# Kernel tuning notes

Hardware: AMD Instinct MI355X
Metric: run time of the kernel (lower is better)

## Reference

```python
import jax, jax.numpy as jnp
import numpy as np

B, L, DIM, K, V = 512, 200, 256, 2048, 100000


def setup_inputs() -> dict:
    key = jax.random.key(0)
    k1, k2, k3, k4, k5 = jax.random.split(key, 5)
    return {
        "history_item_ids": jax.random.randint(k1, (B, L), 0, V, dtype=jnp.int32),
        "history_item_masks": jax.random.randint(k2, (B, L), 0, 3, dtype=jnp.int32),
        "embedding_table": jax.random.normal(k3, (V, DIM), dtype=jnp.float32) * 0.1,
        "code_book": jax.random.normal(k4, (K, DIM), dtype=jnp.float32) * 0.1,
        "W_enc": jax.random.normal(k5, (2 * DIM, DIM), dtype=jnp.float32) * 0.05,
        "b_enc": jnp.zeros((DIM,), dtype=jnp.float32),
    }


def reference(history_item_ids, history_item_masks, embedding_table, code_book, W_enc, b_enc):
    # mask: valid history positions (>= 1)
    mask = (history_item_masks >= 1).astype(jnp.float32)            # [B, L]
    emb = embedding_table[history_item_ids] * mask[:, :, None]      # [B, L, D]
    # masked mean over history (eps matches the tf 1e-9)
    hist_mean = emb.sum(axis=1) / (mask.sum(axis=1, keepdims=True) + 1e-9)  # [B, D]
    # VQ quantization: pairwise squared distances, argmin, codebook gather
    flat = emb.reshape(-1, emb.shape[-1])                           # [B*L, D]
    distances = (
        jnp.sum(flat * flat, axis=1, keepdims=True)
        + jnp.sum(code_book * code_book, axis=1)
        - 2.0 * flat @ code_book.T
    )                                                               # [B*L, K]
    idx = jnp.argmin(distances, axis=1)                             # [B*L]
    vq = code_book[idx].reshape(emb.shape)                          # [B, L, D] (== one_hot @ code_book)
    vq_mean = vq.sum(axis=1) / mask.sum(axis=-1)[:, None]           # [B, D] (no eps in tf vqvae)
    x = jnp.concatenate([vq_mean, hist_mean], axis=-1)              # [B, 2D]
    return x @ W_enc + b_enc                                        # encoder dense -> [B, D]
```

## Files before the change

### kernel.cpp

```cpp
#include <hip/hip_runtime.h>
#include <hip/hip_bf16.h>
#include <cstddef>
#include <cstdint>

#define B_  512
#define L_  200
#define D_  256
#define K_  2048
#define BL_ (B_ * L_)

typedef __bf16 bf16x8 __attribute__((ext_vector_type(8)));
typedef float  f32x16 __attribute__((ext_vector_type(16)));

#define GL_LDS(g, l) __builtin_amdgcn_global_load_lds(                          \
    (const __attribute__((address_space(1))) void*)(g),                         \
    (__attribute__((address_space(3))) void*)(l), 16, 0, 0)

__device__ inline ushort f2bf(float f) {
    union { float f; uint u; } a; a.f = f;
    uint r = a.u + 0x7FFFu + ((a.u >> 16) & 1u);
    return (ushort)(r >> 16);
}

__global__ __launch_bounds__(256) void prep_kernel(const float* __restrict__ cb,
                                                   float* __restrict__ cnorm,
                                                   float* __restrict__ cnormR,
                                                   ushort* __restrict__ cbbf) {
    int code = (blockIdx.x * 256 + threadIdx.x) >> 6;
    int lane = threadIdx.x & 63;
    float4 v = ((const float4*)(cb + (size_t)code * D_))[lane];
    float s = v.x * v.x + v.y * v.y + v.z * v.z + v.w * v.w;
    #pragma unroll
    for (int off = 32; off; off >>= 1) s += __shfl_down(s, off);
    union { ushort us[4]; uint2 u2; } pk;
    pk.us[0] = f2bf(v.x); pk.us[1] = f2bf(v.y); pk.us[2] = f2bf(v.z); pk.us[3] = f2bf(v.w);
    ((uint2*)(cbbf + (size_t)code * D_))[lane] = pk.u2;
    if (lane == 0) {
        cnorm[code] = s;
        int r = code & 31;
        int h = (r >> 2) & 1;
        int j = (r & 3) | ((r >> 3) << 2);
        cnormR[(code & ~31) | (h << 4) | j] = s + 16.0f;
    }
}

struct CN4 { float4 a, b, c, d; };

__device__ inline CN4 ldcn(const float* p) {
    CN4 r;
    r.a = ((const float4*)p)[0];
    r.b = ((const float4*)p)[1];
    r.c = ((const float4*)p)[2];
    r.d = ((const float4*)p)[3];
    return r;
}

#define STAGE(CIDX, BUF) {                                                      \
    int wub = __builtin_amdgcn_readfirstlane((t >> 6) * 512);                   \
    _Pragma("unroll")                                                           \
    for (int i_ = 0; i_ < 8; ++i_) {                                            \
      int slot = wub + i_ * 64 + (t & 63);                                      \
      int n_ = slot >> 5, up_ = slot & 31;                                      \
      int u_ = up_ ^ (n_ & 7);                                                  \
      GL_LDS(cbbf + (((size_t)((cu << 10) + ((CIDX) << 5) + n_)) << 8) + (u_ << 3), \
             (char*)(BUF) + (size_t)(wub + i_ * 64) * 16);                      \
    } }

#define PROCSEL(BUF, NC, CN) {                                                  \
    f32x16 A0, A1;                                                              \
    A0[0]=(CN).a.x; A0[1]=(CN).a.y; A0[2]=(CN).a.z; A0[3]=(CN).a.w;             \
    A0[4]=(CN).b.x; A0[5]=(CN).b.y; A0[6]=(CN).b.z; A0[7]=(CN).b.w;             \
    A0[8]=(CN).c.x; A0[9]=(CN).c.y; A0[10]=(CN).c.z; A0[11]=(CN).c.w;           \
    A0[12]=(CN).d.x; A0[13]=(CN).d.y; A0[14]=(CN).d.z; A0[15]=(CN).d.w;         \
    A1 = A0;                                                                    \
    _Pragma("unroll")                                                           \
    for (int s_ = 0; s_ < 16; ++s_) {                                           \
      bf16x8 aF = *(const bf16x8*)((const char*)(BUF) +                         \
                    (((l31 << 5) + ((2 * s_ + h) ^ swz)) << 4));                \
      A0 = __builtin_amdgcn_mfma_f32_32x32x16_bf16(aF, bfrag[0][s_], A0, 0,0,0);\
      A1 = __builtin_amdgcn_mfma_f32_32x32x16_bf16(aF, bfrag[1][s_], A1, 0,0,0);\
    }                                                                           \
    uint sb_ = (uint)((cu << 10) + ((NC) << 5));                                \
    _Pragma("unroll")                                                           \
    for (int jp_ = 0; jp_ < 8; ++jp_) {                                         \
      int j0_ = 2 * jp_, j1_ = 2 * jp_ + 1;                                     \
      uint c0_ = sb_ + (uint)((j0_ & 3) + 8 * (j0_ >> 2));                      \
      uint c1_ = sb_ + (uint)((j1_ & 3) + 8 * (j1_ >> 2));                      \
      {                                                                         \
        uint ka = (__float_as_uint(A0[j0_]) & 0xFFFFF800u) | (c0_ + h4);        \
        uint kb = (__float_as_uint(A0[j1_]) & 0xFFFFF800u) | (c1_ + h4);        \
        uint lo = min(ka, kb), hi = max(ka, kb);                                \
        uint tt = max(b1a, lo);                                                 \
        b1a = min(b1a, lo);                                                     \
        b2a = min(min(b2a, tt), hi);                                            \
      }                                                                         \
      {                                                                         \
        uint ka = (__float_as_uint(A1[j0_]) & 0xFFFFF800u) | (c0_ + h4);        \
        uint kb = (__float_as_uint(A1[j1_]) & 0xFFFFF800u) | (c1_ + h4);        \
        uint lo = min(ka, kb), hi = max(ka, kb);                                \
        uint tt = max(b1b, lo);                                                 \
        b1b = min(b1b, lo);                                                     \
        b2b = min(min(b2b, tt), hi);                                            \
      }                                                                         \
    } }

__global__ __launch_bounds__(128, 2) void gemm_top2_kernel(
    const int* __restrict__ ids, const int* __restrict__ masks,
    const float* __restrict__ table, const ushort* __restrict__ cbbf,
    const float* __restrict__ cnormR, uint2* __restrict__ cand) {

  __shared__ ushort cbuf0[32 * 256];
  __shared__ ushort cbuf1[32 * 256];

  const int t    = threadIdx.x;
  const int lane = t & 63;
  const int l31  = lane & 31;
  const int h    = lane >> 5;
  const int w    = t >> 6;
  const int ptile = blockIdx.x >> 1;
  const int cu    = blockIdx.x & 1;
  const int swz  = l31 & 7;
  const uint h4  = (uint)(h << 2);

  bf16x8 bfrag[2][16];
  #pragma unroll
  for (int pt = 0; pt < 2; ++pt) {
    int pos = ptile * 128 + w * 64 + pt * 32 + l31;
    int id  = ids[pos];
    float m = (masks[pos] >= 1) ? -2.0f : 0.0f;
    const float* er = table + (size_t)id * D_ + 8 * h;
    #pragma unroll
    for (int s = 0; s < 16; ++s) {
      float4 x = *(const float4*)(er + 16 * s);
      float4 y = *(const float4*)(er + 16 * s + 4);
      bf16x8 b;
      b[0] = (__bf16)(x.x * m); b[1] = (__bf16)(x.y * m);
      b[2] = (__bf16)(x.z * m); b[3] = (__bf16)(x.w * m);
      b[4] = (__bf16)(y.x * m); b[5] = (__bf16)(y.y * m);
      b[6] = (__bf16)(y.z * m); b[7] = (__bf16)(y.w * m);
      bfrag[pt][s] = b;
    }
  }

  uint b1a = 0xFFFFFFFFu, b2a = 0xFFFFFFFFu;
  uint b1b = 0xFFFFFFFFu, b2b = 0xFFFFFFFFu;

  const float* cnh = cnormR + (cu << 10);
  CN4 cnA = ldcn(cnh + 0 * 32 + h * 16);
  STAGE(0, cbuf0);
  __syncthreads();

  #pragma unroll 1
  for (int nc = 0; nc < 32; nc += 2) {
    CN4 cnB = ldcn(cnh + (nc + 1) * 32 + h * 16);
    STAGE(nc + 1, cbuf1);
    PROCSEL(cbuf0, nc, cnA);
    __syncthreads();
    if (nc + 2 < 32) {
      cnA = ldcn(cnh + (nc + 2) * 32 + h * 16);
      STAGE(nc + 2, cbuf0);
    }
    PROCSEL(cbuf1, nc + 1, cnB);
    __syncthreads();
  }

  {
    uint ob1 = __shfl_xor(b1a, 32), ob2 = __shfl_xor(b2a, 32);
    uint m1 = min(b1a, ob1);
    uint m2 = min(min(max(b1a, ob1), b2a), ob2);
    if (h == 0) cand[(size_t)(ptile * 128 + w * 64 + 0 * 32 + l31) * 2 + cu] = make_uint2(m1, m2);
  }
  {
    uint ob1 = __shfl_xor(b1b, 32), ob2 = __shfl_xor(b2b, 32);
    uint m1 = min(b1b, ob1);
    uint m2 = min(min(max(b1b, ob1), b2b), ob2);
    if (h == 0) cand[(size_t)(ptile * 128 + w * 64 + 1 * 32 + l31) * 2 + cu] = make_uint2(m1, m2);
  }
}

#define SEG 5
#define PPB (L_ / SEG)
#define PPW (PPB / 4)

__global__ __launch_bounds__(256) void rescore_accum_kernel(
    const int* __restrict__ ids, const int* __restrict__ masks,
    const float* __restrict__ table, const float* __restrict__ cb,
    const float* __restrict__ cnorm, const uint4* __restrict__ cand,
    float* __restrict__ gacc, int* __restrict__ gcnt) {

    __shared__ float red_vq[4][D_];
    __shared__ float red_e[4][D_];
    __shared__ int   red_c[4];

    const int b   = blockIdx.x / SEG;
    const int seg = blockIdx.x % SEG;
    const int t = threadIdx.x;
    const int wv = t >> 6, lane = t & 63;

    float4 vqa = make_float4(0.f, 0.f, 0.f, 0.f);
    float4 ea  = make_float4(0.f, 0.f, 0.f, 0.f);
    int cnta = 0;

    #pragma unroll 2
    for (int i = 0; i < PPW; ++i) {
        int l = seg * PPB + wv * PPW + i;
        int u = b * L_ + l;
        uint4 k4 = cand[u];
        uint g1 = min(k4.x, k4.z);
        uint g2 = min(min(max(k4.x, k4.z), k4.y), k4.w);
        int ia = (int)(g1 & 0x7FFu), ib2 = (int)(g2 & 0x7FFu);
        int lo = min(ia, ib2), hi = max(ia, ib2);
        int id = ids[u];
        bool mv = (masks[u] >= 1);
        float m = mv ? 1.0f : 0.0f;
        float4 e = ((const float4*)(table + (size_t)id * D_))[lane];
        e.x *= m; e.y *= m; e.z *= m; e.w *= m;
        float4 a  = ((const float4*)(cb + (size_t)lo * D_))[lane];
        float4 bb = ((const float4*)(cb + (size_t)hi * D_))[lane];
        float s1 = fmaf(e.x, a.x,  fmaf(e.y, a.y,  fmaf(e.z, a.z,  e.w * a.w)));
        float s2 = fmaf(e.x, bb.x, fmaf(e.y, bb.y, fmaf(e.z, bb.z, e.w * bb.w)));
        #pragma unroll
        for (int off = 32; off; off >>= 1) {
            s1 += __shfl_xor(s1, off);
            s2 += __shfl_xor(s2, off);
        }
        float d1 = cnorm[lo] - 2.0f * s1;
        float d2 = cnorm[hi] - 2.0f * s2;
        bool sel = (d2 < d1);
        float4 ch = sel ? bb : a;
        vqa.x += ch.x; vqa.y += ch.y; vqa.z += ch.z; vqa.w += ch.w;
        ea.x += e.x; ea.y += e.y; ea.z += e.z; ea.w += e.w;
        cnta += mv ? 1 : 0;
    }

    *(float4*)&red_vq[wv][lane * 4] = vqa;
    *(float4*)&red_e[wv][lane * 4]  = ea;
    if (lane == 0) red_c[wv] = cnta;
    __syncthreads();

    float vs = red_vq[0][t] + red_vq[1][t] + red_vq[2][t] + red_vq[3][t];
    float es = red_e[0][t] + red_e[1][t] + red_e[2][t] + red_e[3][t];
    atomicAdd(&gacc[(size_t)b * (2 * D_) + t], vs);
    atomicAdd(&gacc[(size_t)b * (2 * D_) + D_ + t], es);
    if (t == 0) atomicAdd(&gcnt[b], red_c[0] + red_c[1] + red_c[2] + red_c[3]);
}

__global__ __launch_bounds__(256) void dense_kernel(
    const float* __restrict__ gacc, const int* __restrict__ gcnt,
    const float* __restrict__ W, const float* __restrict__ bvec,
    float* __restrict__ out) {

    __shared__ float x[2 * D_];
    const int b = blockIdx.x;
    const int t = threadIdx.x;

    float fc = (float)gcnt[b];
    x[t]      = gacc[(size_t)b * (2 * D_) + t] / fc;
    x[D_ + t] = gacc[(size_t)b * (2 * D_) + D_ + t] / (fc + 1e-9f);
    __syncthreads();

    float acc = bvec[t];
    #pragma unroll 8
    for (int i = 0; i < 2 * D_; ++i)
        acc = fmaf(x[i], W[i * D_ + t], acc);
    out[(size_t)b * D_ + t] = acc;
}

extern "C" void kernel_launch(void* const* d_in, const int* in_sizes, int n_in,
                              void* d_out, int out_size, void* d_ws, size_t ws_size,
                              hipStream_t stream) {
    const int*   ids   = (const int*)  d_in[0];
    const int*   masks = (const int*)  d_in[1];
    const float* table = (const float*)d_in[2];
    const float* cb    = (const float*)d_in[3];
    const float* W     = (const float*)d_in[4];
    const float* bvec  = (const float*)d_in[5];
    float* out = (float*)d_out;

    char* p = (char*)d_ws;
    float*  cnorm  = (float*)p;             p += 8192;
    float*  cnormR = (float*)p;             p += 8192;
    ushort* cbbf   = (ushort*)p;            p += 1048576;
    uint2*  cand   = (uint2*)p;             p += (size_t)BL_ * 16;
    float*  gacc   = (float*)p;             p += (size_t)B_ * 2 * D_ * 4;
    int*    gcnt   = (int*)p;               p += B_ * 4;

    hipMemsetAsync(gacc, 0, (size_t)B_ * 2 * D_ * 4 + B_ * 4, stream);

    prep_kernel<<<K_ * 64 / 256, 256, 0, stream>>>(cb, cnorm, cnormR, cbbf);
    gemm_top2_kernel<<<(BL_ / 128) * 2, 128, 0, stream>>>(ids, masks, table, cbbf, cnormR, cand);
    rescore_accum_kernel<<<B_ * SEG, 256, 0, stream>>>(ids, masks, table, cb, cnorm,
                                                       (const uint4*)cand, gacc, gcnt);
    dense_kernel<<<B_, 256, 0, stream>>>(gacc, gcnt, W, bvec, out);
}
```

Measured before the change: 333.5 us.

## Load MFMA codebook fragments directly from global in prepacked layout, dropping LDS staging

The prep kernel now writes the bf16 codebook in a layout that matches the MFMA A-fragment order, one 16-byte load per lane. The GEMM kernel then double-buffers these fragments in registers straight from global/L2, replacing the LDS double-buffer, the async global-to-LDS copies and the per-chunk __syncthreads. The goal is to remove LDS round-trips and barrier stalls, at the cost of more VGPR pressure and exposed global/L2 latency per chunk. Separately, the rescore kernel splits each batch row into 10 segments instead of 5 and fully unrolls its inner loop for more parallelism. The final prefetch iteration reads past each half's codebook region, but those values are never used.

```diff
diff --git a/kernel.cpp b/kernel.cpp
--- a/kernel.cpp
+++ b/kernel.cpp
@@ -12,10 +12,6 @@
 typedef __bf16 bf16x8 __attribute__((ext_vector_type(8)));
 typedef float  f32x16 __attribute__((ext_vector_type(16)));
 
-#define GL_LDS(g, l) __builtin_amdgcn_global_load_lds(                          \
-    (const __attribute__((address_space(1))) void*)(g),                         \
-    (__attribute__((address_space(3))) void*)(l), 16, 0, 0)
-
 __device__ inline ushort f2bf(float f) {
     union { float f; uint u; } a; a.f = f;
     uint r = a.u + 0x7FFFu + ((a.u >> 16) & 1u);
@@ -25,7 +21,7 @@
 __global__ __launch_bounds__(256) void prep_kernel(const float* __restrict__ cb,
                                                    float* __restrict__ cnorm,
                                                    float* __restrict__ cnormR,
-                                                   ushort* __restrict__ cbbf) {
+                                                   char* __restrict__ cbbfA) {
     int code = (blockIdx.x * 256 + threadIdx.x) >> 6;
     int lane = threadIdx.x & 63;
     float4 v = ((const float4*)(cb + (size_t)code * D_))[lane];
@@ -34,7 +30,10 @@
     for (int off = 32; off; off >>= 1) s += __shfl_down(s, off);
     union { ushort us[4]; uint2 u2; } pk;
     pk.us[0] = f2bf(v.x); pk.us[1] = f2bf(v.y); pk.us[2] = f2bf(v.z); pk.us[3] = f2bf(v.w);
-    ((uint2*)(cbbf + (size_t)code * D_))[lane] = pk.u2;
+    size_t off8 = (size_t)(code >> 5) * 16384 + (size_t)(lane >> 2) * 1024
+                + (size_t)((lane >> 1) & 1) * 512 + (size_t)(code & 31) * 16
+                + (size_t)(lane & 1) * 8;
+    *(uint2*)(cbbfA + off8) = pk.u2;
     if (lane == 0) {
         cnorm[code] = s;
         int r = code & 31;
@@ -55,62 +54,10 @@
     return r;
 }
 
-#define STAGE(CIDX, BUF) {                                                      \
-    int wub = __builtin_amdgcn_readfirstlane((t >> 6) * 512);                   \
-    _Pragma("unroll")                                                           \
-    for (int i_ = 0; i_ < 8; ++i_) {                                            \
-      int slot = wub + i_ * 64 + (t & 63);                                      \
-      int n_ = slot >> 5, up_ = slot & 31;                                      \
-      int u_ = up_ ^ (n_ & 7);                                                  \
-      GL_LDS(cbbf + (((size_t)((cu << 10) + ((CIDX) << 5) + n_)) << 8) + (u_ << 3), \
-             (char*)(BUF) + (size_t)(wub + i_ * 64) * 16);                      \
-    } }
-
-#define PROCSEL(BUF, NC, CN) {                                                  \
-    f32x16 A0, A1;                                                              \
-    A0[0]=(CN).a.x; A0[1]=(CN).a.y; A0[2]=(CN).a.z; A0[3]=(CN).a.w;             \
-    A0[4]=(CN).b.x; A0[5]=(CN).b.y; A0[6]=(CN).b.z; A0[7]=(CN).b.w;             \
-    A0[8]=(CN).c.x; A0[9]=(CN).c.y; A0[10]=(CN).c.z; A0[11]=(CN).c.w;           \
-    A0[12]=(CN).d.x; A0[13]=(CN).d.y; A0[14]=(CN).d.z; A0[15]=(CN).d.w;         \
-    A1 = A0;                                                                    \
-    _Pragma("unroll")                                                           \
-    for (int s_ = 0; s_ < 16; ++s_) {                                           \
-      bf16x8 aF = *(const bf16x8*)((const char*)(BUF) +                         \
-                    (((l31 << 5) + ((2 * s_ + h) ^ swz)) << 4));                \
-      A0 = __builtin_amdgcn_mfma_f32_32x32x16_bf16(aF, bfrag[0][s_], A0, 0,0,0);\
-      A1 = __builtin_amdgcn_mfma_f32_32x32x16_bf16(aF, bfrag[1][s_], A1, 0,0,0);\
-    }                                                                           \
-    uint sb_ = (uint)((cu << 10) + ((NC) << 5));                                \
-    _Pragma("unroll")                                                           \
-    for (int jp_ = 0; jp_ < 8; ++jp_) {                                         \
-      int j0_ = 2 * jp_, j1_ = 2 * jp_ + 1;                                     \
-      uint c0_ = sb_ + (uint)((j0_ & 3) + 8 * (j0_ >> 2));                      \
-      uint c1_ = sb_ + (uint)((j1_ & 3) + 8 * (j1_ >> 2));                      \
-      {                                                                         \
-        uint ka = (__float_as_uint(A0[j0_]) & 0xFFFFF800u) | (c0_ + h4);        \
-        uint kb = (__float_as_uint(A0[j1_]) & 0xFFFFF800u) | (c1_ + h4);        \
-        uint lo = min(ka, kb), hi = max(ka, kb);                                \
-        uint tt = max(b1a, lo);                                                 \
-        b1a = min(b1a, lo);                                                     \
-        b2a = min(min(b2a, tt), hi);                                            \
-      }                                                                         \
-      {                                                                         \
-        uint ka = (__float_as_uint(A1[j0_]) & 0xFFFFF800u) | (c0_ + h4);        \
-        uint kb = (__float_as_uint(A1[j1_]) & 0xFFFFF800u) | (c1_ + h4);        \
-        uint lo = min(ka, kb), hi = max(ka, kb);                                \
-        uint tt = max(b1b, lo);                                                 \
-        b1b = min(b1b, lo);                                                     \
-        b2b = min(min(b2b, tt), hi);                                            \
-      }                                                                         \
-    } }
-
 __global__ __launch_bounds__(128, 2) void gemm_top2_kernel(
     const int* __restrict__ ids, const int* __restrict__ masks,
-    const float* __restrict__ table, const ushort* __restrict__ cbbf,
+    const float* __restrict__ table, const char* __restrict__ cbbfA,
     const float* __restrict__ cnormR, uint2* __restrict__ cand) {
-
-  __shared__ ushort cbuf0[32 * 256];
-  __shared__ ushort cbuf1[32 * 256];
 
   const int t    = threadIdx.x;
   const int lane = t & 63;
@@ -119,7 +66,6 @@
   const int w    = t >> 6;
   const int ptile = blockIdx.x >> 1;
   const int cu    = blockIdx.x & 1;
-  const int swz  = l31 & 7;
   const uint h4  = (uint)(h << 2);
 
   bf16x8 bfrag[2][16];
@@ -145,23 +91,70 @@
   uint b1a = 0xFFFFFFFFu, b2a = 0xFFFFFFFFu;
   uint b1b = 0xFFFFFFFFu, b2b = 0xFFFFFFFFu;
 
+  const char* base = cbbfA + (size_t)cu * (32 * 16384);
+  const int lane16 = lane * 16;
   const float* cnh = cnormR + (cu << 10);
-  CN4 cnA = ldcn(cnh + 0 * 32 + h * 16);
-  STAGE(0, cbuf0);
-  __syncthreads();
+
+  bf16x8 buf0[8], buf1[8];
+  #pragma unroll
+  for (int i = 0; i < 8; ++i)
+    buf0[i] = *(const bf16x8*)(base + i * 1024 + lane16);
+  #pragma unroll
+  for (int i = 0; i < 8; ++i)
+    buf1[i] = *(const bf16x8*)(base + 8192 + i * 1024 + lane16);
+  CN4 cnbuf = ldcn(cnh + h * 16);
 
   #pragma unroll 1
-  for (int nc = 0; nc < 32; nc += 2) {
-    CN4 cnB = ldcn(cnh + (nc + 1) * 32 + h * 16);
-    STAGE(nc + 1, cbuf1);
-    PROCSEL(cbuf0, nc, cnA);
-    __syncthreads();
-    if (nc + 2 < 32) {
-      cnA = ldcn(cnh + (nc + 2) * 32 + h * 16);
-      STAGE(nc + 2, cbuf0);
-    }
-    PROCSEL(cbuf1, nc + 1, cnB);
-    __syncthreads();
+  for (int nc = 0; nc < 32; ++nc) {
+    f32x16 A0, A1;
+    A0[0]=cnbuf.a.x; A0[1]=cnbuf.a.y; A0[2]=cnbuf.a.z; A0[3]=cnbuf.a.w;
+    A0[4]=cnbuf.b.x; A0[5]=cnbuf.b.y; A0[6]=cnbuf.b.z; A0[7]=cnbuf.b.w;
+    A0[8]=cnbuf.c.x; A0[9]=cnbuf.c.y; A0[10]=cnbuf.c.z; A0[11]=cnbuf.c.w;
+    A0[12]=cnbuf.d.x; A0[13]=cnbuf.d.y; A0[14]=cnbuf.d.z; A0[15]=cnbuf.d.w;
+    A1 = A0;
+    cnbuf = ldcn(cnh + (nc + 1) * 32 + h * 16);
+
+    #pragma unroll
+    for (int i = 0; i < 8; ++i) {
+      A0 = __builtin_amdgcn_mfma_f32_32x32x16_bf16(buf0[i], bfrag[0][i], A0, 0, 0, 0);
+      A1 = __builtin_amdgcn_mfma_f32_32x32x16_bf16(buf0[i], bfrag[1][i], A1, 0, 0, 0);
+    }
+    #pragma unroll
+    for (int i = 0; i < 8; ++i)
+      buf0[i] = *(const bf16x8*)(base + (size_t)(2 * nc + 2) * 8192 + i * 1024 + lane16);
+
+    #pragma unroll
+    for (int i = 0; i < 8; ++i) {
+      A0 = __builtin_amdgcn_mfma_f32_32x32x16_bf16(buf1[i], bfrag[0][8 + i], A0, 0, 0, 0);
+      A1 = __builtin_amdgcn_mfma_f32_32x32x16_bf16(buf1[i], bfrag[1][8 + i], A1, 0, 0, 0);
+    }
+    #pragma unroll
+    for (int i = 0; i < 8; ++i)
+      buf1[i] = *(const bf16x8*)(base + (size_t)(2 * nc + 3) * 8192 + i * 1024 + lane16);
+
+    uint sb = (uint)((cu << 10) + (nc << 5));
+    #pragma unroll
+    for (int jp = 0; jp < 8; ++jp) {
+      int j0 = 2 * jp, j1 = 2 * jp + 1;
+      uint c0 = sb + (uint)((j0 & 3) + 8 * (j0 >> 2)) + h4;
+      uint c1 = sb + (uint)((j1 & 3) + 8 * (j1 >> 2)) + h4;
+      {
+        uint ka = (__float_as_uint(A0[j0]) & 0xFFFFF800u) | c0;
+        uint kb = (__float_as_uint(A0[j1]) & 0xFFFFF800u) | c1;
+        uint lo = min(ka, kb), hi = max(ka, kb);
+        uint tt = max(b1a, lo);
+        b1a = min(b1a, lo);
+        b2a = min(min(b2a, tt), hi);
+      }
+      {
+        uint ka = (__float_as_uint(A1[j0]) & 0xFFFFF800u) | c0;
+        uint kb = (__float_as_uint(A1[j1]) & 0xFFFFF800u) | c1;
+        uint lo = min(ka, kb), hi = max(ka, kb);
+        uint tt = max(b1b, lo);
+        b1b = min(b1b, lo);
+        b2b = min(min(b2b, tt), hi);
+      }
+    }
   }
 
   {
@@ -178,7 +171,7 @@
   }
 }
 
-#define SEG 5
+#define SEG 10
 #define PPB (L_ / SEG)
 #define PPW (PPB / 4)
 
@@ -201,7 +194,7 @@
     float4 ea  = make_float4(0.f, 0.f, 0.f, 0.f);
     int cnta = 0;
 
-    #pragma unroll 2
+    #pragma unroll
     for (int i = 0; i < PPW; ++i) {
         int l = seg * PPB + wv * PPW + i;
         int u = b * L_ + l;
@@ -280,15 +273,15 @@
     char* p = (char*)d_ws;
     float*  cnorm  = (float*)p;             p += 8192;
     float*  cnormR = (float*)p;             p += 8192;
-    ushort* cbbf   = (ushort*)p;            p += 1048576;
+    char*   cbbfA  = p;                     p += 1048576;
     uint2*  cand   = (uint2*)p;             p += (size_t)BL_ * 16;
     float*  gacc   = (float*)p;             p += (size_t)B_ * 2 * D_ * 4;
     int*    gcnt   = (int*)p;               p += B_ * 4;
 
     hipMemsetAsync(gacc, 0, (size_t)B_ * 2 * D_ * 4 + B_ * 4, stream);
 
-    prep_kernel<<<K_ * 64 / 256, 256, 0, stream>>>(cb, cnorm, cnormR, cbbf);
-    gemm_top2_kernel<<<(BL_ / 128) * 2, 128, 0, stream>>>(ids, masks, table, cbbf, cnormR, cand);
+    prep_kernel<<<K_ * 64 / 256, 256, 0, stream>>>(cb, cnorm, cnormR, cbbfA);
+    gemm_top2_kernel<<<(BL_ / 128) * 2, 128, 0, stream>>>(ids, masks, table, cbbfA, cnormR, cand);
     rescore_accum_kernel<<<B_ * SEG, 256, 0, stream>>>(ids, masks, table, cb, cnorm,
                                                        (const uint4*)cand, gacc, gcnt);
     dense_kernel<<<B_, 256, 0, stream>>>(gacc, gcnt, W, bvec, out);
```

Result: slower. 389.1 us (+16.7%).

## Split codebook into four slices with cheaper per-lane min and 8-candidate rescoring

Applied to the files above, without the earlier changes.

The GEMM/top-k kernel now uses 256-thread blocks covering 256 positions and splits the codebook into four 512-code slices instead of two 1024-code slices. Each slice's running top-2 selection per lane is replaced by two running minima over disjoint column groups, combined into a top-2 after the cross-half shuffle. The rescore kernel then exactly re-evaluates 8 candidates per position (4 slices × 2) in fp32 instead of 2, and uses twice as many segments per batch row. This cuts the ALU selection cost in the MFMA loop and increases block-level parallelism. In exchange, the candidate buffer doubles in size and the rescore pass does four times as many codebook row gathers and reductions.

```diff
diff --git a/kernel.cpp b/kernel.cpp
--- a/kernel.cpp
+++ b/kernel.cpp
@@ -8,6 +8,8 @@
 #define D_  256
 #define K_  2048
 #define BL_ (B_ * L_)
+#define CUS 4
+#define NCH 16
 
 typedef __bf16 bf16x8 __attribute__((ext_vector_type(8)));
 typedef float  f32x16 __attribute__((ext_vector_type(16)));
@@ -56,13 +58,13 @@
 }
 
 #define STAGE(CIDX, BUF) {                                                      \
-    int wub = __builtin_amdgcn_readfirstlane((t >> 6) * 512);                   \
+    int wub = __builtin_amdgcn_readfirstlane((t >> 6) * 256);                   \
     _Pragma("unroll")                                                           \
-    for (int i_ = 0; i_ < 8; ++i_) {                                            \
+    for (int i_ = 0; i_ < 4; ++i_) {                                            \
       int slot = wub + i_ * 64 + (t & 63);                                      \
       int n_ = slot >> 5, up_ = slot & 31;                                      \
       int u_ = up_ ^ (n_ & 7);                                                  \
-      GL_LDS(cbbf + (((size_t)((cu << 10) + ((CIDX) << 5) + n_)) << 8) + (u_ << 3), \
+      GL_LDS(cbbf + (((size_t)((cu << 9) + ((CIDX) << 5) + n_)) << 8) + (u_ << 3), \
              (char*)(BUF) + (size_t)(wub + i_ * 64) * 16);                      \
     } }
 
@@ -80,31 +82,17 @@
       A0 = __builtin_amdgcn_mfma_f32_32x32x16_bf16(aF, bfrag[0][s_], A0, 0,0,0);\
       A1 = __builtin_amdgcn_mfma_f32_32x32x16_bf16(aF, bfrag[1][s_], A1, 0,0,0);\
     }                                                                           \
-    uint sb_ = (uint)((cu << 10) + ((NC) << 5));                                \
+    uint kbase = (uint)((cu << 9) | ((NC) << 5)) | h4;                          \
     _Pragma("unroll")                                                           \
-    for (int jp_ = 0; jp_ < 8; ++jp_) {                                         \
-      int j0_ = 2 * jp_, j1_ = 2 * jp_ + 1;                                     \
-      uint c0_ = sb_ + (uint)((j0_ & 3) + 8 * (j0_ >> 2));                      \
-      uint c1_ = sb_ + (uint)((j1_ & 3) + 8 * (j1_ >> 2));                      \
-      {                                                                         \
-        uint ka = (__float_as_uint(A0[j0_]) & 0xFFFFF800u) | (c0_ + h4);        \
-        uint kb = (__float_as_uint(A0[j1_]) & 0xFFFFF800u) | (c1_ + h4);        \
-        uint lo = min(ka, kb), hi = max(ka, kb);                                \
-        uint tt = max(b1a, lo);                                                 \
-        b1a = min(b1a, lo);                                                     \
-        b2a = min(min(b2a, tt), hi);                                            \
-      }                                                                         \
-      {                                                                         \
-        uint ka = (__float_as_uint(A1[j0_]) & 0xFFFFF800u) | (c0_ + h4);        \
-        uint kb = (__float_as_uint(A1[j1_]) & 0xFFFFF800u) | (c1_ + h4);        \
-        uint lo = min(ka, kb), hi = max(ka, kb);                                \
-        uint tt = max(b1b, lo);                                                 \
-        b1b = min(b1b, lo);                                                     \
-        b2b = min(min(b2b, tt), hi);                                            \
-      }                                                                         \
+    for (int j_ = 0; j_ < 16; ++j_) {                                           \
+      uint idx_ = kbase | (uint)((j_ & 3) + 8 * (j_ >> 2));                     \
+      uint k0_ = (__float_as_uint(A0[j_]) & 0xFFFFF800u) | idx_;                \
+      uint k1_ = (__float_as_uint(A1[j_]) & 0xFFFFF800u) | idx_;                \
+      if (j_ < 8) { g0a = min(g0a, k0_); g0b = min(g0b, k1_); }                 \
+      else        { g1a = min(g1a, k0_); g1b = min(g1b, k1_); }                 \
     } }
 
-__global__ __launch_bounds__(128, 2) void gemm_top2_kernel(
+__global__ __launch_bounds__(256, 2) void gemm_top2_kernel(
     const int* __restrict__ ids, const int* __restrict__ masks,
     const float* __restrict__ table, const ushort* __restrict__ cbbf,
     const float* __restrict__ cnormR, uint2* __restrict__ cand) {
@@ -117,15 +105,15 @@
   const int l31  = lane & 31;
   const int h    = lane >> 5;
   const int w    = t >> 6;
-  const int ptile = blockIdx.x >> 1;
-  const int cu    = blockIdx.x & 1;
+  const int ptile = blockIdx.x >> 2;
+  const int cu    = blockIdx.x & 3;
   const int swz  = l31 & 7;
   const uint h4  = (uint)(h << 2);
 
   bf16x8 bfrag[2][16];
   #pragma unroll
   for (int pt = 0; pt < 2; ++pt) {
-    int pos = ptile * 128 + w * 64 + pt * 32 + l31;
+    int pos = ptile * 256 + w * 64 + pt * 32 + l31;
     int id  = ids[pos];
     float m = (masks[pos] >= 1) ? -2.0f : 0.0f;
     const float* er = table + (size_t)id * D_ + 8 * h;
@@ -142,21 +130,21 @@
     }
   }
 
-  uint b1a = 0xFFFFFFFFu, b2a = 0xFFFFFFFFu;
-  uint b1b = 0xFFFFFFFFu, b2b = 0xFFFFFFFFu;
-
-  const float* cnh = cnormR + (cu << 10);
-  CN4 cnA = ldcn(cnh + 0 * 32 + h * 16);
+  uint g0a = 0xFFFFFFFFu, g1a = 0xFFFFFFFFu;
+  uint g0b = 0xFFFFFFFFu, g1b = 0xFFFFFFFFu;
+
+  const float* cnh = cnormR + (cu << 9);
+  CN4 cnA = ldcn(cnh + h * 16);
   STAGE(0, cbuf0);
   __syncthreads();
 
   #pragma unroll 1
-  for (int nc = 0; nc < 32; nc += 2) {
+  for (int nc = 0; nc < NCH; nc += 2) {
     CN4 cnB = ldcn(cnh + (nc + 1) * 32 + h * 16);
     STAGE(nc + 1, cbuf1);
     PROCSEL(cbuf0, nc, cnA);
     __syncthreads();
-    if (nc + 2 < 32) {
+    if (nc + 2 < NCH) {
       cnA = ldcn(cnh + (nc + 2) * 32 + h * 16);
       STAGE(nc + 2, cbuf0);
     }
@@ -164,28 +152,29 @@
     __syncthreads();
   }
 
-  {
-    uint ob1 = __shfl_xor(b1a, 32), ob2 = __shfl_xor(b2a, 32);
-    uint m1 = min(b1a, ob1);
-    uint m2 = min(min(max(b1a, ob1), b2a), ob2);
-    if (h == 0) cand[(size_t)(ptile * 128 + w * 64 + 0 * 32 + l31) * 2 + cu] = make_uint2(m1, m2);
+  #pragma unroll
+  for (int pt = 0; pt < 2; ++pt) {
+    uint x0 = pt ? g0b : g0a;
+    uint x1 = pt ? g1b : g1a;
+    uint o0 = __shfl_xor(x0, 32);
+    uint o1 = __shfl_xor(x1, 32);
+    uint a = min(x0, o0), A = max(x0, o0);
+    uint b = min(x1, o1), B = max(x1, o1);
+    uint m1 = min(a, b);
+    uint m2 = min(max(a, b), min(A, B));
+    int pos = ptile * 256 + w * 64 + pt * 32 + l31;
+    if (h == 0) cand[(size_t)pos * 4 + cu] = make_uint2(m1, m2);
   }
-  {
-    uint ob1 = __shfl_xor(b1b, 32), ob2 = __shfl_xor(b2b, 32);
-    uint m1 = min(b1b, ob1);
-    uint m2 = min(min(max(b1b, ob1), b2b), ob2);
-    if (h == 0) cand[(size_t)(ptile * 128 + w * 64 + 1 * 32 + l31) * 2 + cu] = make_uint2(m1, m2);
-  }
-}
-
-#define SEG 5
+}
+
+#define SEG 10
 #define PPB (L_ / SEG)
 #define PPW (PPB / 4)
 
 __global__ __launch_bounds__(256) void rescore_accum_kernel(
     const int* __restrict__ ids, const int* __restrict__ masks,
     const float* __restrict__ table, const float* __restrict__ cb,
-    const float* __restrict__ cnorm, const uint4* __restrict__ cand,
+    const float* __restrict__ cnorm, const uint4* __restrict__ cand4,
     float* __restrict__ gacc, int* __restrict__ gcnt) {
 
     __shared__ float red_vq[4][D_];
@@ -201,33 +190,48 @@
     float4 ea  = make_float4(0.f, 0.f, 0.f, 0.f);
     int cnta = 0;
 
-    #pragma unroll 2
+    #pragma unroll 1
     for (int i = 0; i < PPW; ++i) {
         int l = seg * PPB + wv * PPW + i;
         int u = b * L_ + l;
-        uint4 k4 = cand[u];
-        uint g1 = min(k4.x, k4.z);
-        uint g2 = min(min(max(k4.x, k4.z), k4.y), k4.w);
-        int ia = (int)(g1 & 0x7FFu), ib2 = (int)(g2 & 0x7FFu);
-        int lo = min(ia, ib2), hi = max(ia, ib2);
+        uint4 ka = cand4[2 * u];
+        uint4 kb = cand4[2 * u + 1];
+        int k[8];
+        k[0] = (int)(ka.x & 0x7FFu); k[1] = (int)(ka.y & 0x7FFu);
+        k[2] = (int)(ka.z & 0x7FFu); k[3] = (int)(ka.w & 0x7FFu);
+        k[4] = (int)(kb.x & 0x7FFu); k[5] = (int)(kb.y & 0x7FFu);
+        k[6] = (int)(kb.z & 0x7FFu); k[7] = (int)(kb.w & 0x7FFu);
+
         int id = ids[u];
         bool mv = (masks[u] >= 1);
         float m = mv ? 1.0f : 0.0f;
         float4 e = ((const float4*)(table + (size_t)id * D_))[lane];
         e.x *= m; e.y *= m; e.z *= m; e.w *= m;
-        float4 a  = ((const float4*)(cb + (size_t)lo * D_))[lane];
-        float4 bb = ((const float4*)(cb + (size_t)hi * D_))[lane];
-        float s1 = fmaf(e.x, a.x,  fmaf(e.y, a.y,  fmaf(e.z, a.z,  e.w * a.w)));
-        float s2 = fmaf(e.x, bb.x, fmaf(e.y, bb.y, fmaf(e.z, bb.z, e.w * bb.w)));
+
+        float4 c[8];
+        float  s[8];
+        #pragma unroll
+        for (int q = 0; q < 8; ++q) {
+            c[q] = ((const float4*)(cb + (size_t)k[q] * D_))[lane];
+            s[q] = fmaf(e.x, c[q].x, fmaf(e.y, c[q].y, fmaf(e.z, c[q].z, e.w * c[q].w)));
+        }
         #pragma unroll
         for (int off = 32; off; off >>= 1) {
-            s1 += __shfl_xor(s1, off);
-            s2 += __shfl_xor(s2, off);
+            #pragma unroll
+            for (int q = 0; q < 8; ++q) s[q] += __shfl_xor(s[q], off);
         }
-        float d1 = cnorm[lo] - 2.0f * s1;
-        float d2 = cnorm[hi] - 2.0f * s2;
-        bool sel = (d2 < d1);
-        float4 ch = sel ? bb : a;
+
+        float bs = cnorm[k[0]] - 2.0f * s[0];
+        int   bk = k[0];
+        float4 ch = c[0];
+        #pragma unroll
+        for (int q = 1; q < 8; ++q) {
+            float sc = cnorm[k[q]] - 2.0f * s[q];
+            bool better = (sc < bs) || (sc == bs && k[q] < bk);
+            bs = better ? sc : bs;
+            bk = better ? k[q] : bk;
+            ch = better ? c[q] : ch;
+        }
         vqa.x += ch.x; vqa.y += ch.y; vqa.z += ch.z; vqa.w += ch.w;
         ea.x += e.x; ea.y += e.y; ea.z += e.z; ea.w += e.w;
         cnta += mv ? 1 : 0;
@@ -281,14 +285,14 @@
     float*  cnorm  = (float*)p;             p += 8192;
     float*  cnormR = (float*)p;             p += 8192;
     ushort* cbbf   = (ushort*)p;            p += 1048576;
-    uint2*  cand   = (uint2*)p;             p += (size_t)BL_ * 16;
+    uint2*  cand   = (uint2*)p;             p += (size_t)BL_ * 4 * 8;
     float*  gacc   = (float*)p;             p += (size_t)B_ * 2 * D_ * 4;
     int*    gcnt   = (int*)p;               p += B_ * 4;
 
     hipMemsetAsync(gacc, 0, (size_t)B_ * 2 * D_ * 4 + B_ * 4, stream);
 
     prep_kernel<<<K_ * 64 / 256, 256, 0, stream>>>(cb, cnorm, cnormR, cbbf);
-    gemm_top2_kernel<<<(BL_ / 128) * 2, 128, 0, stream>>>(ids, masks, table, cbbf, cnormR, cand);
+    gemm_top2_kernel<<<(BL_ / 256) * CUS, 256, 0, stream>>>(ids, masks, table, cbbf, cnormR, cand);
     rescore_accum_kernel<<<B_ * SEG, 256, 0, stream>>>(ids, masks, table, cb, cnorm,
                                                        (const uint4*)cand, gacc, gcnt);
     dense_kernel<<<B_, 256, 0, stream>>>(gacc, gcnt, W, bvec, out);
```

New measurement: 705.8 us. 112% more time.

## Fuse top-2 rescoring and masked accumulation into the MFMA distance kernel

Applied to the files above, without the earlier changes.

The separate rescore/accumulate kernel is merged into the GEMM top-2 kernel. Each block now scans all 2048 codes itself instead of splitting the codebook across two blocks, so no candidate keys need a cross-block merge. The block exact-rescores its 128 positions' two candidates from shared memory, then sums the chosen codewords and masked embeddings per batch row (at most two rows per block) with global atomics. This removes the candidate buffer round-trip and one kernel launch. The cost is half as many GEMM blocks, each doing twice the work, which risks worse load balance and occupancy across CUs, plus a less parallel epilogue inside each block.

```diff
diff --git a/kernel.cpp b/kernel.cpp
--- a/kernel.cpp
+++ b/kernel.cpp
@@ -62,7 +62,7 @@
       int slot = wub + i_ * 64 + (t & 63);                                      \
       int n_ = slot >> 5, up_ = slot & 31;                                      \
       int u_ = up_ ^ (n_ & 7);                                                  \
-      GL_LDS(cbbf + (((size_t)((cu << 10) + ((CIDX) << 5) + n_)) << 8) + (u_ << 3), \
+      GL_LDS(cbbf + (((size_t)(((CIDX) << 5) + n_)) << 8) + (u_ << 3),          \
              (char*)(BUF) + (size_t)(wub + i_ * 64) * 16);                      \
     } }
 
@@ -80,23 +80,23 @@
       A0 = __builtin_amdgcn_mfma_f32_32x32x16_bf16(aF, bfrag[0][s_], A0, 0,0,0);\
       A1 = __builtin_amdgcn_mfma_f32_32x32x16_bf16(aF, bfrag[1][s_], A1, 0,0,0);\
     }                                                                           \
-    uint sb_ = (uint)((cu << 10) + ((NC) << 5));                                \
+    uint kbase = ((uint)(NC) << 5) | h4;                                        \
     _Pragma("unroll")                                                           \
     for (int jp_ = 0; jp_ < 8; ++jp_) {                                         \
       int j0_ = 2 * jp_, j1_ = 2 * jp_ + 1;                                     \
-      uint c0_ = sb_ + (uint)((j0_ & 3) + 8 * (j0_ >> 2));                      \
-      uint c1_ = sb_ + (uint)((j1_ & 3) + 8 * (j1_ >> 2));                      \
+      uint c0_ = kbase + (uint)((j0_ & 3) + 8 * (j0_ >> 2));                    \
+      uint c1_ = kbase + (uint)((j1_ & 3) + 8 * (j1_ >> 2));                    \
       {                                                                         \
-        uint ka = (__float_as_uint(A0[j0_]) & 0xFFFFF800u) | (c0_ + h4);        \
-        uint kb = (__float_as_uint(A0[j1_]) & 0xFFFFF800u) | (c1_ + h4);        \
+        uint ka = (__float_as_uint(A0[j0_]) & 0xFFFFF800u) | c0_;               \
+        uint kb = (__float_as_uint(A0[j1_]) & 0xFFFFF800u) | c1_;               \
         uint lo = min(ka, kb), hi = max(ka, kb);                                \
         uint tt = max(b1a, lo);                                                 \
         b1a = min(b1a, lo);                                                     \
         b2a = min(min(b2a, tt), hi);                                            \
       }                                                                         \
       {                                                                         \
-        uint ka = (__float_as_uint(A1[j0_]) & 0xFFFFF800u) | (c0_ + h4);        \
-        uint kb = (__float_as_uint(A1[j1_]) & 0xFFFFF800u) | (c1_ + h4);        \
+        uint ka = (__float_as_uint(A1[j0_]) & 0xFFFFF800u) | c0_;               \
+        uint kb = (__float_as_uint(A1[j1_]) & 0xFFFFF800u) | c1_;               \
         uint lo = min(ka, kb), hi = max(ka, kb);                                \
         uint tt = max(b1b, lo);                                                 \
         b1b = min(b1b, lo);                                                     \
@@ -104,30 +104,41 @@
       }                                                                         \
     } }
 
-__global__ __launch_bounds__(128, 2) void gemm_top2_kernel(
+__global__ __launch_bounds__(128, 2) void gemm_fused_kernel(
     const int* __restrict__ ids, const int* __restrict__ masks,
     const float* __restrict__ table, const ushort* __restrict__ cbbf,
-    const float* __restrict__ cnormR, uint2* __restrict__ cand) {
+    const float* __restrict__ cnormR, const float* __restrict__ cnorm,
+    const float* __restrict__ cb,
+    float* __restrict__ gacc, int* __restrict__ gcnt) {
 
   __shared__ ushort cbuf0[32 * 256];
   __shared__ ushort cbuf1[32 * 256];
+  __shared__ uint  key1s[128], key2s[128];
+  __shared__ int   ids_s[128];
+  __shared__ float mask_s[128];
+  __shared__ int   qidx_s[128];
+  __shared__ int   cnt01[2];
 
   const int t    = threadIdx.x;
   const int lane = t & 63;
   const int l31  = lane & 31;
   const int h    = lane >> 5;
   const int w    = t >> 6;
-  const int ptile = blockIdx.x >> 1;
-  const int cu    = blockIdx.x & 1;
+  const int P0   = blockIdx.x * 128;
   const int swz  = l31 & 7;
   const uint h4  = (uint)(h << 2);
+
+  if (t < 2) cnt01[t] = 0;
 
   bf16x8 bfrag[2][16];
   #pragma unroll
   for (int pt = 0; pt < 2; ++pt) {
-    int pos = ptile * 128 + w * 64 + pt * 32 + l31;
+    int pl  = w * 64 + pt * 32 + l31;
+    int pos = P0 + pl;
     int id  = ids[pos];
-    float m = (masks[pos] >= 1) ? -2.0f : 0.0f;
+    bool mv = (masks[pos] >= 1);
+    if (h == 0) { ids_s[pl] = id; mask_s[pl] = mv ? 1.0f : 0.0f; }
+    float m = mv ? -2.0f : 0.0f;
     const float* er = table + (size_t)id * D_ + 8 * h;
     #pragma unroll
     for (int s = 0; s < 16; ++s) {
@@ -145,104 +156,116 @@
   uint b1a = 0xFFFFFFFFu, b2a = 0xFFFFFFFFu;
   uint b1b = 0xFFFFFFFFu, b2b = 0xFFFFFFFFu;
 
-  const float* cnh = cnormR + (cu << 10);
-  CN4 cnA = ldcn(cnh + 0 * 32 + h * 16);
   STAGE(0, cbuf0);
   __syncthreads();
+  CN4 cnA = ldcn(cnormR + h * 16);
 
   #pragma unroll 1
-  for (int nc = 0; nc < 32; nc += 2) {
-    CN4 cnB = ldcn(cnh + (nc + 1) * 32 + h * 16);
+  for (int nc = 0; nc < 64; nc += 2) {
+    CN4 cnB = ldcn(cnormR + (nc + 1) * 32 + h * 16);
     STAGE(nc + 1, cbuf1);
     PROCSEL(cbuf0, nc, cnA);
     __syncthreads();
-    if (nc + 2 < 32) {
-      cnA = ldcn(cnh + (nc + 2) * 32 + h * 16);
+    if (nc + 2 < 64) {
+      cnA = ldcn(cnormR + (nc + 2) * 32 + h * 16);
       STAGE(nc + 2, cbuf0);
     }
     PROCSEL(cbuf1, nc + 1, cnB);
     __syncthreads();
   }
 
+  #pragma unroll
+  for (int pt = 0; pt < 2; ++pt) {
+    uint x1 = pt ? b1b : b1a;
+    uint x2 = pt ? b2b : b2a;
+    uint o1 = __shfl_xor(x1, 32);
+    uint o2 = __shfl_xor(x2, 32);
+    uint m1 = min(x1, o1);
+    uint m2 = min(min(max(x1, o1), x2), o2);
+    int pl = w * 64 + pt * 32 + l31;
+    if (h == 0) { key1s[pl] = m1; key2s[pl] = m2; }
+  }
+  __syncthreads();
+
+  #pragma unroll 1
+  for (int g = 0; g < 4; ++g) {
+    int pl  = w * 64 + g * 16 + (lane >> 2);
+    int sub = lane & 3;
+    int k1 = (int)(key1s[pl] & 0x7FFu);
+    int k2 = (int)(key2s[pl] & 0x7FFu);
+    int id = ids_s[pl];
+    float m = mask_s[pl];
+    const float4* ep  = (const float4*)(table + (size_t)id * D_ + sub * 64);
+    const float4* c1p = (const float4*)(cb + (size_t)k1 * D_ + sub * 64);
+    const float4* c2p = (const float4*)(cb + (size_t)k2 * D_ + sub * 64);
+    float d1 = 0.f, d2 = 0.f;
+    #pragma unroll
+    for (int i = 0; i < 16; ++i) {
+      float4 e = ep[i];
+      float4 a = c1p[i];
+      float4 b = c2p[i];
+      d1 = fmaf(e.x, a.x, fmaf(e.y, a.y, fmaf(e.z, a.z, fmaf(e.w, a.w, d1))));
+      d2 = fmaf(e.x, b.x, fmaf(e.y, b.y, fmaf(e.z, b.z, fmaf(e.w, b.w, d2))));
+    }
+    d1 += __shfl_xor(d1, 1); d1 += __shfl_xor(d1, 2);
+    d2 += __shfl_xor(d2, 1); d2 += __shfl_xor(d2, 2);
+    if (sub == 0) {
+      float s1 = cnorm[k1] - 2.0f * m * d1;
+      float s2 = cnorm[k2] - 2.0f * m * d2;
+      qidx_s[pl] = (s2 < s1 || (s2 == s1 && k2 < k1)) ? k2 : k1;
+    }
+  }
+  __syncthreads();
+
+  const int bA = P0 / L_;
+  const int bB = bA + 1;
+  int split = (bA + 1) * L_ - P0;
+  if (split > 128) split = 128;
+
+  float2 vq0 = {0.f, 0.f}, e0 = {0.f, 0.f};
+  float2 vq1 = {0.f, 0.f}, e1 = {0.f, 0.f};
+
+  #pragma unroll 4
+  for (int l = 0; l < split; ++l) {
+    int q = qidx_s[l]; int idl = ids_s[l]; float ml = mask_s[l];
+    float2 cv = *(const float2*)(cb + (size_t)q * D_ + 2 * t);
+    float2 ev = *(const float2*)(table + (size_t)idl * D_ + 2 * t);
+    vq0.x += cv.x; vq0.y += cv.y;
+    e0.x = fmaf(ml, ev.x, e0.x); e0.y = fmaf(ml, ev.y, e0.y);
+  }
+  #pragma unroll 4
+  for (int l = split; l < 128; ++l) {
+    int q = qidx_s[l]; int idl = ids_s[l]; float ml = mask_s[l];
+    float2 cv = *(const float2*)(cb + (size_t)q * D_ + 2 * t);
+    float2 ev = *(const float2*)(table + (size_t)idl * D_ + 2 * t);
+    vq1.x += cv.x; vq1.y += cv.y;
+    e1.x = fmaf(ml, ev.x, e1.x); e1.y = fmaf(ml, ev.y, e1.y);
+  }
+
   {
-    uint ob1 = __shfl_xor(b1a, 32), ob2 = __shfl_xor(b2a, 32);
-    uint m1 = min(b1a, ob1);
-    uint m2 = min(min(max(b1a, ob1), b2a), ob2);
-    if (h == 0) cand[(size_t)(ptile * 128 + w * 64 + 0 * 32 + l31) * 2 + cu] = make_uint2(m1, m2);
-  }
+    int p1 = (t >= split) ? 1 : 0;
+    if (mask_s[t] != 0.f) atomicAdd(&cnt01[p1], 1);
+  }
+  __syncthreads();
+
   {
-    uint ob1 = __shfl_xor(b1b, 32), ob2 = __shfl_xor(b2b, 32);
-    uint m1 = min(b1b, ob1);
-    uint m2 = min(min(max(b1b, ob1), b2b), ob2);
-    if (h == 0) cand[(size_t)(ptile * 128 + w * 64 + 1 * 32 + l31) * 2 + cu] = make_uint2(m1, m2);
-  }
-}
-
-#define SEG 5
-#define PPB (L_ / SEG)
-#define PPW (PPB / 4)
-
-__global__ __launch_bounds__(256) void rescore_accum_kernel(
-    const int* __restrict__ ids, const int* __restrict__ masks,
-    const float* __restrict__ table, const float* __restrict__ cb,
-    const float* __restrict__ cnorm, const uint4* __restrict__ cand,
-    float* __restrict__ gacc, int* __restrict__ gcnt) {
-
-    __shared__ float red_vq[4][D_];
-    __shared__ float red_e[4][D_];
-    __shared__ int   red_c[4];
-
-    const int b   = blockIdx.x / SEG;
-    const int seg = blockIdx.x % SEG;
-    const int t = threadIdx.x;
-    const int wv = t >> 6, lane = t & 63;
-
-    float4 vqa = make_float4(0.f, 0.f, 0.f, 0.f);
-    float4 ea  = make_float4(0.f, 0.f, 0.f, 0.f);
-    int cnta = 0;
-
-    #pragma unroll 2
-    for (int i = 0; i < PPW; ++i) {
-        int l = seg * PPB + wv * PPW + i;
-        int u = b * L_ + l;
-        uint4 k4 = cand[u];
-        uint g1 = min(k4.x, k4.z);
-        uint g2 = min(min(max(k4.x, k4.z), k4.y), k4.w);
-        int ia = (int)(g1 & 0x7FFu), ib2 = (int)(g2 & 0x7FFu);
-        int lo = min(ia, ib2), hi = max(ia, ib2);
-        int id = ids[u];
-        bool mv = (masks[u] >= 1);
-        float m = mv ? 1.0f : 0.0f;
-        float4 e = ((const float4*)(table + (size_t)id * D_))[lane];
-        e.x *= m; e.y *= m; e.z *= m; e.w *= m;
-        float4 a  = ((const float4*)(cb + (size_t)lo * D_))[lane];
-        float4 bb = ((const float4*)(cb + (size_t)hi * D_))[lane];
-        float s1 = fmaf(e.x, a.x,  fmaf(e.y, a.y,  fmaf(e.z, a.z,  e.w * a.w)));
-        float s2 = fmaf(e.x, bb.x, fmaf(e.y, bb.y, fmaf(e.z, bb.z, e.w * bb.w)));
-        #pragma unroll
-        for (int off = 32; off; off >>= 1) {
-            s1 += __shfl_xor(s1, off);
-            s2 += __shfl_xor(s2, off);
-        }
-        float d1 = cnorm[lo] - 2.0f * s1;
-        float d2 = cnorm[hi] - 2.0f * s2;
-        bool sel = (d2 < d1);
-        float4 ch = sel ? bb : a;
-        vqa.x += ch.x; vqa.y += ch.y; vqa.z += ch.z; vqa.w += ch.w;
-        ea.x += e.x; ea.y += e.y; ea.z += e.z; ea.w += e.w;
-        cnta += mv ? 1 : 0;
-    }
-
-    *(float4*)&red_vq[wv][lane * 4] = vqa;
-    *(float4*)&red_e[wv][lane * 4]  = ea;
-    if (lane == 0) red_c[wv] = cnta;
-    __syncthreads();
-
-    float vs = red_vq[0][t] + red_vq[1][t] + red_vq[2][t] + red_vq[3][t];
-    float es = red_e[0][t] + red_e[1][t] + red_e[2][t] + red_e[3][t];
-    atomicAdd(&gacc[(size_t)b * (2 * D_) + t], vs);
-    atomicAdd(&gacc[(size_t)b * (2 * D_) + D_ + t], es);
-    if (t == 0) atomicAdd(&gcnt[b], red_c[0] + red_c[1] + red_c[2] + red_c[3]);
+    float* g0 = gacc + (size_t)bA * (2 * D_);
+    atomicAdd(g0 + 2 * t,            vq0.x);
+    atomicAdd(g0 + 2 * t + 1,        vq0.y);
+    atomicAdd(g0 + D_ + 2 * t,       e0.x);
+    atomicAdd(g0 + D_ + 2 * t + 1,   e0.y);
+    if (split < 128) {
+      float* g1 = gacc + (size_t)bB * (2 * D_);
+      atomicAdd(g1 + 2 * t,          vq1.x);
+      atomicAdd(g1 + 2 * t + 1,      vq1.y);
+      atomicAdd(g1 + D_ + 2 * t,     e1.x);
+      atomicAdd(g1 + D_ + 2 * t + 1, e1.y);
+    }
+    if (t == 0) {
+      atomicAdd(&gcnt[bA], cnt01[0]);
+      if (split < 128) atomicAdd(&gcnt[bB], cnt01[1]);
+    }
+  }
 }
 
 __global__ __launch_bounds__(256) void dense_kernel(
@@ -281,15 +304,13 @@
     float*  cnorm  = (float*)p;             p += 8192;
     float*  cnormR = (float*)p;             p += 8192;
     ushort* cbbf   = (ushort*)p;            p += 1048576;
-    uint2*  cand   = (uint2*)p;             p += (size_t)BL_ * 16;
     float*  gacc   = (float*)p;             p += (size_t)B_ * 2 * D_ * 4;
     int*    gcnt   = (int*)p;               p += B_ * 4;
 
     hipMemsetAsync(gacc, 0, (size_t)B_ * 2 * D_ * 4 + B_ * 4, stream);
 
     prep_kernel<<<K_ * 64 / 256, 256, 0, stream>>>(cb, cnorm, cnormR, cbbf);
-    gemm_top2_kernel<<<(BL_ / 128) * 2, 128, 0, stream>>>(ids, masks, table, cbbf, cnormR, cand);
-    rescore_accum_kernel<<<B_ * SEG, 256, 0, stream>>>(ids, masks, table, cb, cnorm,
-                                                       (const uint4*)cand, gacc, gcnt);
+    gemm_fused_kernel<<<BL_ / 128, 128, 0, stream>>>(ids, masks, table, cbbf, cnormR,
+                                                     cnorm, cb, gacc, gcnt);
     dense_kernel<<<B_, 256, 0, stream>>>(gacc, gcnt, W, bvec, out);
 }
```

After: 357.8 us. 7.3% more time.
